# Optimization experiments

Measured on AMD Instinct MI355X. Metric: run time of the kernel, lower is better.

## Reference

```python
import jax, jax.numpy as jnp
import numpy as np

K = 8192      # codebook_dim
D = 256       # embedding_dim
BETA = 0.25
DECAY = 0.99
EPS = 1e-05


def setup_inputs() -> dict:
    key = jax.random.key(0)
    k1, k2, k3, k4 = jax.random.split(key, 4)
    lim = 1.0 / K
    return {
        "z": jax.random.normal(k1, (8, D, 32, 32), dtype=jnp.float32),
        "embedding": jax.random.uniform(k2, (K, D), minval=-lim, maxval=lim, dtype=jnp.float32),
        "cluster_size": jax.random.uniform(k3, (K,), dtype=jnp.float32),
        "ema_w": jax.random.uniform(k4, (K, D), minval=-lim, maxval=lim, dtype=jnp.float32),
    }


def reference(z, embedding, cluster_size, ema_w):
    # z: [B, C, H, W] -> [B, H, W, C]
    zp = jnp.transpose(z, (0, 2, 3, 1))
    zf = zp.reshape(-1, D)                                  # [N, D]
    # squared L2 distance to each code: ||z||^2 + ||e||^2 - 2 z.e
    d = (jnp.sum(zf * zf, axis=1, keepdims=True)
         + jnp.sum(embedding * embedding, axis=1)
         - 2.0 * jnp.einsum("nd,kd->nk", zf, embedding))    # [N, K]
    idx = jnp.argmin(d, axis=1)                             # [N]
    z_q = embedding[idx].reshape(zp.shape)                  # [B, H, W, C]

    # EMA update (training branch), expressed with segment sums instead of
    # materializing the one-hot [N, K] matrix.
    counts = jax.ops.segment_sum(jnp.ones_like(idx, dtype=zf.dtype), idx, num_segments=K)
    new_cs = cluster_size * DECAY + (1.0 - DECAY) * counts
    n = jnp.sum(new_cs)
    new_cs = (new_cs + EPS) / (n + K * EPS) * n
    dw = jax.ops.segment_sum(zf, idx, num_segments=K)       # encodings.T @ zf
    new_ema_w = ema_w * DECAY + (1.0 - DECAY) * dw
    new_embedding = new_ema_w / new_cs[:, None]

    sg = jax.lax.stop_gradient
    loss = jnp.mean((sg(z_q) - zp) ** 2) + BETA * jnp.mean((z_q - sg(zp)) ** 2)
    # straight-through estimator, back to NCHW
    z_q_out = jnp.transpose(zp + sg(z_q - zp), (0, 3, 1, 2))
    return z_q_out, loss, idx, new_cs, new_ema_w, new_embedding
```

## Files before the change

kernel.cpp:

```cpp
#include <hip/hip_runtime.h>

#define CHW 262144
#define HWD 1024

typedef _Float16 v8h __attribute__((ext_vector_type(8)));
typedef _Float16 v4h __attribute__((ext_vector_type(4)));
typedef float    v4f __attribute__((ext_vector_type(4)));

static const unsigned OFF_ASQ  = 0;
static const unsigned OFF_BSQ  = 8192;
static const unsigned OFF_CNT  = 16384;
static const unsigned OFF_HEAD = 24576;
static const unsigned OFF_NXT  = 32768;
static const unsigned OFF_SCAL = 40960;
static const unsigned OFF_AH   = 40968;
static const unsigned OFF_AM   = 1089544;
static const unsigned OFF_BH   = 2138120;
static const unsigned OFF_BM   = 3186696;

#define GLL(g, l) __builtin_amdgcn_global_load_lds( \
    (const __attribute__((address_space(1))) void*)(g), \
    (__attribute__((address_space(3))) void*)(l), 16, 0, 0)

__global__ __launch_bounds__(256) void k_prep(const float* __restrict__ z,
        const float* __restrict__ emb, float* __restrict__ asq, float* __restrict__ bsq,
        _Float16* __restrict__ Bh, _Float16* __restrict__ Bm,
        _Float16* __restrict__ Ah, _Float16* __restrict__ Am,
        float* __restrict__ zerobase) {
    int bx = blockIdx.x;
    int t = threadIdx.x;
    if (bx < 32) {
        int n = bx * 256 + t;
        const float* p = z + (size_t)(n >> 10) * CHW + (n & 1023);
        float s = 0.f;
        #pragma unroll 8
        for (int c = 0; c < 256; ++c) { float v = p[(size_t)c << 10]; s = fmaf(v, v, s); }
        asq[n] = s;
    } else if (bx < 2080) {
        int w = (bx - 32) * 4 + (t >> 6);
        int lane = t & 63;
        float4 v = *(const float4*)(emb + (size_t)w * 256 + lane * 4);
        float s = v.x * v.x;
        s = fmaf(v.y, v.y, s); s = fmaf(v.z, v.z, s); s = fmaf(v.w, v.w, s);
        #pragma unroll
        for (int m = 1; m < 64; m <<= 1) s += __shfl_xor(s, m, 64);
        if (lane == 0) bsq[w] = s;
        float e0 = v.x * 8192.0f, e1 = v.y * 8192.0f, e2 = v.z * 8192.0f, e3 = v.w * 8192.0f;
        _Float16 h0 = (_Float16)e0, h1 = (_Float16)e1, h2 = (_Float16)e2, h3 = (_Float16)e3;
        v4h hv = {h0, h1, h2, h3};
        v4h mv = {(_Float16)((e0 - (float)h0) * 2048.0f),
                  (_Float16)((e1 - (float)h1) * 2048.0f),
                  (_Float16)((e2 - (float)h2) * 2048.0f),
                  (_Float16)((e3 - (float)h3) * 2048.0f)};
        *(v4h*)(Bh + (size_t)w * 256 + lane * 4) = hv;
        *(v4h*)(Bm + (size_t)w * 256 + lane * 4) = mv;
    } else if (bx < 2592) {
        __shared__ float s[64][65];
        int blk = bx - 2080;
        int hw0 = (blk & 15) * 64;
        int c0  = ((blk >> 4) & 3) * 64;
        int b   = blk >> 6;
        #pragma unroll
        for (int ii = 0; ii < 16; ++ii) {
            int e = t + ii * 256;
            int c = e >> 6, x = e & 63;
            s[c][x] = z[(size_t)b * CHW + (size_t)(c0 + c) * HWD + hw0 + x];
        }
        __syncthreads();
        int n = t & 63, cseg = (t >> 6) * 16;
        _Float16 hbuf[16], mbuf[16];
        #pragma unroll
        for (int j = 0; j < 16; ++j) {
            float v = s[cseg + j][n];
            _Float16 h = (_Float16)v;
            float r = v - (float)h;
            hbuf[j] = h;
            mbuf[j] = (_Float16)(r * 2048.0f);
        }
        size_t off = ((size_t)b * 1024 + hw0 + n) * 256 + c0 + cseg;
        *(v8h*)(Ah + off)     = *(v8h*)(hbuf);
        *(v8h*)(Ah + off + 8) = *(v8h*)(hbuf + 8);
        *(v8h*)(Am + off)     = *(v8h*)(mbuf);
        *(v8h*)(Am + off + 8) = *(v8h*)(mbuf + 8);
    } else {
        int idx = (bx - 2592) * 1024 + t * 4;
        *(float4*)(zerobase + idx) = (float4){0.f, 0.f, 0.f, 0.f};
        if (bx == 2592 && t == 0)
            *(float4*)(zerobase + 24576) = (float4){0.f, 0.f, 0.f, 0.f};
    }
}

__global__ __launch_bounds__(512, 4) void k_main(
        const _Float16* __restrict__ Ah, const _Float16* __restrict__ Am,
        const _Float16* __restrict__ Bh, const _Float16* __restrict__ Bm,
        const float* __restrict__ asq, const float* __restrict__ bsq,
        unsigned* __restrict__ pdk) {
    __shared__ _Float16 lds[32768];
    const int kt = blockIdx.x, nt = blockIdx.y;
    const int n0 = nt * 128, k0 = kt * 128;
    const int t = threadIdx.x;
    const int lane = t & 63, w = t >> 6;
    const int wrow = w >> 1, wcol = w & 1;
    const int lm = lane & 15, quad = lane >> 4;

    v4f acc1[2][4], acc2[2][4];
    #pragma unroll
    for (int i = 0; i < 2; ++i)
        #pragma unroll
        for (int j = 0; j < 4; ++j) { acc1[i][j] = (v4f){0.f,0.f,0.f,0.f}; acc2[i][j] = (v4f){0.f,0.f,0.f,0.f}; }

    const int row0 = t >> 2;
    const int c40 = (t & 3) ^ ((row0 >> 1) & 3);
    const char* gA  = (const char*)Ah + (size_t)(n0 + row0) * 512 + c40 * 16;
    const char* gAm = (const char*)Am + (size_t)(n0 + row0) * 512 + c40 * 16;
    const char* gB  = (const char*)Bh + (size_t)(k0 + row0) * 512 + c40 * 16;
    const char* gBm = (const char*)Bm + (size_t)(k0 + row0) * 512 + c40 * 16;

    int sa[2], sb[4];
    #pragma unroll
    for (int i = 0; i < 2; ++i) {
        int mr = wrow * 32 + i * 16 + lm;
        sa[i] = mr * 32 + ((quad ^ ((mr >> 1) & 3)) * 8);
    }
    #pragma unroll
    for (int j = 0; j < 4; ++j) {
        int nr = wcol * 64 + j * 16 + lm;
        sb[j] = nr * 32 + ((quad ^ ((nr >> 1) & 3)) * 8);
    }

    auto stage = [&](int cb, int buf) {
        const size_t co = (size_t)cb * 64;
        _Float16* l = lds + buf * 16384 + t * 8;
        GLL(gA + co,  l);
        GLL(gAm + co, l + 4096);
        GLL(gB + co,  l + 8192);
        GLL(gBm + co, l + 12288);
    };

    stage(0, 0);
    for (int cb = 0; cb < 8; ++cb) {
        __syncthreads();
        if (cb < 7) stage(cb + 1, (cb + 1) & 1);
        const _Float16* L = lds + (cb & 1) * 16384;

        v8h fa[2], fam[2];
        #pragma unroll
        for (int i = 0; i < 2; ++i) {
            fa[i]  = *(const v8h*)(L + sa[i]);
            fam[i] = *(const v8h*)(L + 4096 + sa[i]);
        }
        #pragma unroll
        for (int jh = 0; jh < 2; ++jh) {
            v8h fb0  = *(const v8h*)(L + 8192 + sb[jh * 2]);
            v8h fb1  = *(const v8h*)(L + 8192 + sb[jh * 2 + 1]);
            v8h fbm0 = *(const v8h*)(L + 12288 + sb[jh * 2]);
            v8h fbm1 = *(const v8h*)(L + 12288 + sb[jh * 2 + 1]);
            #pragma unroll
            for (int i = 0; i < 2; ++i) {
                int j0 = jh * 2;
                acc1[i][j0]     = __builtin_amdgcn_mfma_f32_16x16x32_f16(fa[i],  fb0,  acc1[i][j0], 0, 0, 0);
                acc2[i][j0]     = __builtin_amdgcn_mfma_f32_16x16x32_f16(fa[i],  fbm0, acc2[i][j0], 0, 0, 0);
                acc2[i][j0]     = __builtin_amdgcn_mfma_f32_16x16x32_f16(fam[i], fb0,  acc2[i][j0], 0, 0, 0);
                acc1[i][j0 + 1] = __builtin_amdgcn_mfma_f32_16x16x32_f16(fa[i],  fb1,  acc1[i][j0 + 1], 0, 0, 0);
                acc2[i][j0 + 1] = __builtin_amdgcn_mfma_f32_16x16x32_f16(fa[i],  fbm1, acc2[i][j0 + 1], 0, 0, 0);
                acc2[i][j0 + 1] = __builtin_amdgcn_mfma_f32_16x16x32_f16(fam[i], fb1,  acc2[i][j0 + 1], 0, 0, 0);
            }
        }
    }

    float bvv[4];
    #pragma unroll
    for (int j = 0; j < 4; ++j) bvv[j] = bsq[k0 + wcol * 64 + j * 16 + lm];
    __syncthreads();
    unsigned* lrow = (unsigned*)lds;
    #pragma unroll
    for (int i = 0; i < 2; ++i) {
        #pragma unroll
        for (int r = 0; r < 4; ++r) {
            int mm = wrow * 32 + i * 16 + quad * 4 + r;
            float av_ = asq[n0 + mm];
            unsigned best = 0xFFFFFFFFu;
            #pragma unroll
            for (int j = 0; j < 4; ++j) {
                float S = fmaf(acc2[i][j][r], 4.8828125e-4f, acc1[i][j][r]) * 1.220703125e-4f;
                float dd = (av_ + bvv[j]) - 2.0f * S;
                float gv = dd - av_;
                int mi = (int)(gv * 65536.0f) + 32768;
                int col = k0 + wcol * 64 + j * 16 + lm;
                unsigned key = ((unsigned)mi << 13) | (unsigned)col;
                best = key < best ? key : best;
            }
            #pragma unroll
            for (int xm = 1; xm < 16; xm <<= 1) {
                unsigned o = __shfl_xor(best, xm, 64);
                best = o < best ? o : best;
            }
            if (lm == 0) lrow[wcol * 128 + mm] = best;
        }
    }
    __syncthreads();
    if (t < 256) pdk[(((size_t)nt * 128 + kt * 2) << 7) + t] = lrow[t];
}

__global__ __launch_bounds__(256) void k_zqr(const unsigned* __restrict__ pdk,
        const float* __restrict__ z, const float* __restrict__ emb, const float* __restrict__ cs,
        float* __restrict__ out_idx, int* __restrict__ cnt,
        int* __restrict__ head, int* __restrict__ nxt,
        float* __restrict__ out_zq, float* __restrict__ scal) {
    const int bx = blockIdx.x, by = blockIdx.y;
    const int n0 = bx * 64, c00 = by * 64;
    const int lane = threadIdx.x & 63, g = threadIdx.x >> 6;
    const int nt = bx >> 1, mb = (bx & 1) * 64;

    unsigned mn = 0xFFFFFFFFu;
    const unsigned* base = pdk + (((size_t)nt * 128 + g * 32) << 7) + mb + lane;
    #pragma unroll 8
    for (int jj = 0; jj < 32; ++jj) {
        unsigned key = base[jj << 7];
        mn = key < mn ? key : mn;
    }
    __shared__ unsigned part[4][64];
    part[g][lane] = mn;
    __syncthreads();
    unsigned k0v = part[0][lane], k1v = part[1][lane];
    unsigned k2v = part[2][lane], k3v = part[3][lane];
    unsigned f01 = k0v < k1v ? k0v : k1v;
    unsigned f23 = k2v < k3v ? k2v : k3v;
    unsigned fkey = f01 < f23 ? f01 : f23;
    int idxn = (int)(fkey & 8191u);
    int n = n0 + lane;

    if (by == 0) {
        if (g == 0) {
            out_idx[n] = (float)idxn;
            atomicAdd(cnt + idxn, 1);
            int old = atomicExch(head + idxn, n + 1);
            nxt[n] = old;
        } else if (g == 1) {
            float cv = cs[n];
            #pragma unroll
            for (int m = 1; m < 64; m <<= 1) cv += __shfl_xor(cv, m, 64);
            if (lane == 0) atomicAdd(scal + 1, cv);
        }
    }

    int b = n >> 10, hw = n & 1023;
    const float* zr = z + (size_t)b * CHW + hw;
    const float* er = emb + (size_t)idxn * 256;
    float* oz = out_zq + (size_t)b * CHW + hw;
    float ls = 0.f;
    #pragma unroll
    for (int q = 0; q < 4; ++q) {
        int c = c00 + g * 16 + q * 4;
        float4 e4 = *(const float4*)(er + c);
        float ev[4] = {e4.x, e4.y, e4.z, e4.w};
        #pragma unroll
        for (int r = 0; r < 4; ++r) {
            float zp = zr[(size_t)(c + r) << 10];
            float dif = ev[r] - zp;
            oz[(size_t)(c + r) << 10] = zp + dif;
            ls = fmaf(dif, dif, ls);
        }
    }
    #pragma unroll
    for (int m = 1; m < 64; m <<= 1) ls += __shfl_xor(ls, m, 64);
    __shared__ float red[4];
    if (lane == 0) red[g] = ls;
    __syncthreads();
    if (threadIdx.x == 0) atomicAdd(scal, red[0] + red[1] + red[2] + red[3]);
}

__global__ __launch_bounds__(256) void k_fin(const float* __restrict__ cs, const float* __restrict__ ema,
        const int* __restrict__ head, const int* __restrict__ nxt,
        const _Float16* __restrict__ Ah, const _Float16* __restrict__ Am,
        const float* __restrict__ scal, const int* __restrict__ cnt,
        float* __restrict__ out_ncs, float* __restrict__ out_ema,
        float* __restrict__ out_emb, float* __restrict__ out_loss) {
    int k = blockIdx.x * 4 + (threadIdx.x >> 6);
    int lane = threadIdx.x & 63;
    float4 dwv = {0.f, 0.f, 0.f, 0.f};
    int cur = head[k];
    while (cur) {
        int n = cur - 1;
        v4h hh = *(const v4h*)(Ah + (size_t)n * 256 + lane * 4);
        v4h mm = *(const v4h*)(Am + (size_t)n * 256 + lane * 4);
        dwv.x += fmaf((float)mm[0], 4.8828125e-4f, (float)hh[0]);
        dwv.y += fmaf((float)mm[1], 4.8828125e-4f, (float)hh[1]);
        dwv.z += fmaf((float)mm[2], 4.8828125e-4f, (float)hh[2]);
        dwv.w += fmaf((float)mm[3], 4.8828125e-4f, (float)hh[3]);
        cur = nxt[n];
    }
    const float C1 = (float)(1.0 - 0.99);
    const float KEPS = (float)(8192 * 1e-5);
    float ncs0v = cs[k] * 0.99f + C1 * (float)cnt[k];
    float nsum = 0.99f * scal[1] + C1 * 8192.0f;
    float ncs = (ncs0v + 1e-5f) / (nsum + KEPS) * nsum;
    if (lane == 0) out_ncs[k] = ncs;
    size_t base = (size_t)k * 256 + lane * 4;
    float4 e4 = *(const float4*)(ema + base);
    float r0 = e4.x * 0.99f + C1 * dwv.x;
    float r1 = e4.y * 0.99f + C1 * dwv.y;
    float r2 = e4.z * 0.99f + C1 * dwv.z;
    float r3 = e4.w * 0.99f + C1 * dwv.w;
    out_ema[base + 0] = r0; out_ema[base + 1] = r1; out_ema[base + 2] = r2; out_ema[base + 3] = r3;
    out_emb[base + 0] = r0 / ncs; out_emb[base + 1] = r1 / ncs;
    out_emb[base + 2] = r2 / ncs; out_emb[base + 3] = r3 / ncs;
    if (blockIdx.x == 0 && threadIdx.x == 0) {
        float m = scal[0] * (1.0f / 2097152.0f);
        out_loss[0] = m + 0.25f * m;
    }
}

extern "C" void kernel_launch(void* const* d_in, const int* in_sizes, int n_in,
                              void* d_out, int out_size, void* d_ws, size_t ws_size,
                              hipStream_t stream) {
    const float* z   = (const float*)d_in[0];
    const float* emb = (const float*)d_in[1];
    const float* cs  = (const float*)d_in[2];
    const float* ema = (const float*)d_in[3];
    float* out = (float*)d_out;
    float* wsf = (float*)d_ws;

    float* asq  = wsf + OFF_ASQ;
    float* bsq  = wsf + OFF_BSQ;
    int*   cnt  = (int*)(wsf + OFF_CNT);
    int*   head = (int*)(wsf + OFF_HEAD);
    int*   nxt  = (int*)(wsf + OFF_NXT);
    float* scal = wsf + OFF_SCAL;
    _Float16* Ah = (_Float16*)(wsf + OFF_AH);
    _Float16* Am = (_Float16*)(wsf + OFF_AM);
    _Float16* Bh = (_Float16*)(wsf + OFF_BH);
    _Float16* Bm = (_Float16*)(wsf + OFF_BM);

    float* out_zq   = out;
    float* out_loss = out + 2097152;
    float* out_idx  = out + 2097153;
    float* out_ncs  = out + 2105345;
    float* out_ema  = out + 2113537;
    float* out_emb  = out + 4210689;

    unsigned* pdk = (unsigned*)(out + 2113540);

    k_prep<<<2608, 256, 0, stream>>>(z, emb, asq, bsq, Bh, Bm, Ah, Am, wsf + OFF_CNT);
    k_main<<<dim3(64, 64), 512, 0, stream>>>(Ah, Am, Bh, Bm, asq, bsq, pdk);
    k_zqr<<<dim3(128, 4), 256, 0, stream>>>(pdk, z, emb, cs, out_idx, cnt, head, nxt, out_zq, scal);
    k_fin<<<2048, 256, 0, stream>>>(cs, ema, head, nxt, Ah, Am, scal, cnt, out_ncs, out_ema, out_emb, out_loss);
}
```

Measured before the change: 242.3 us.

## Halve k_main block to 4 waves with 64x64 per-wave tiles

Cuts k_main from 512 to 256 threads per 128x128 tile, so each wave computes a 64x64 sub-tile (4x4 MFMA fragments) instead of 32x64. Each thread now issues two global-to-LDS loads per operand. The change raises register reuse of A/B fragments per LDS read and cuts LDS traffic per FLOP. It also swaps __syncthreads for an explicit vmcnt wait plus barrier, and adds sched_barrier/setprio grouping to interleave LDS reads with MFMA bursts. The cost is more accumulator registers and fewer waves per CU to hide latency.

```diff
diff --git a/kernel.cpp b/kernel.cpp
--- a/kernel.cpp
+++ b/kernel.cpp
@@ -90,7 +90,7 @@
     }
 }
 
-__global__ __launch_bounds__(512, 4) void k_main(
+__global__ __launch_bounds__(256, 2) void k_main(
         const _Float16* __restrict__ Ah, const _Float16* __restrict__ Am,
         const _Float16* __restrict__ Bh, const _Float16* __restrict__ Bm,
         const float* __restrict__ asq, const float* __restrict__ bsq,
@@ -103,9 +103,9 @@
     const int wrow = w >> 1, wcol = w & 1;
     const int lm = lane & 15, quad = lane >> 4;
 
-    v4f acc1[2][4], acc2[2][4];
-    #pragma unroll
-    for (int i = 0; i < 2; ++i)
+    v4f acc1[4][4], acc2[4][4];
+    #pragma unroll
+    for (int i = 0; i < 4; ++i)
         #pragma unroll
         for (int j = 0; j < 4; ++j) { acc1[i][j] = (v4f){0.f,0.f,0.f,0.f}; acc2[i][j] = (v4f){0.f,0.f,0.f,0.f}; }
 
@@ -116,10 +116,10 @@
     const char* gB  = (const char*)Bh + (size_t)(k0 + row0) * 512 + c40 * 16;
     const char* gBm = (const char*)Bm + (size_t)(k0 + row0) * 512 + c40 * 16;
 
-    int sa[2], sb[4];
-    #pragma unroll
-    for (int i = 0; i < 2; ++i) {
-        int mr = wrow * 32 + i * 16 + lm;
+    int sa[4], sb[4];
+    #pragma unroll
+    for (int i = 0; i < 4; ++i) {
+        int mr = wrow * 64 + i * 16 + lm;
         sa[i] = mr * 32 + ((quad ^ ((mr >> 1) & 3)) * 8);
     }
     #pragma unroll
@@ -131,42 +131,81 @@
     auto stage = [&](int cb, int buf) {
         const size_t co = (size_t)cb * 64;
         _Float16* l = lds + buf * 16384 + t * 8;
-        GLL(gA + co,  l);
-        GLL(gAm + co, l + 4096);
-        GLL(gB + co,  l + 8192);
-        GLL(gBm + co, l + 12288);
+        GLL(gA + co,           l);
+        GLL(gA + co + 32768,   l + 2048);
+        GLL(gAm + co,          l + 4096);
+        GLL(gAm + co + 32768,  l + 6144);
+        GLL(gB + co,           l + 8192);
+        GLL(gB + co + 32768,   l + 10240);
+        GLL(gBm + co,          l + 12288);
+        GLL(gBm + co + 32768,  l + 14336);
     };
+
+#define MFMA16(A, B, C) __builtin_amdgcn_mfma_f32_16x16x32_f16(A, B, C, 0, 0, 0)
+#define PROD(I, J, FA, FAM, FB, FBM) do { \
+        acc1[I][J] = MFMA16(FA,  FB,  acc1[I][J]); \
+        acc2[I][J] = MFMA16(FA,  FBM, acc2[I][J]); \
+        acc2[I][J] = MFMA16(FAM, FB,  acc2[I][J]); \
+    } while (0)
 
     stage(0, 0);
     for (int cb = 0; cb < 8; ++cb) {
-        __syncthreads();
+        asm volatile("s_waitcnt vmcnt(0)" ::: "memory");
+        __builtin_amdgcn_s_barrier();
+        __builtin_amdgcn_sched_barrier(0);
         if (cb < 7) stage(cb + 1, (cb + 1) & 1);
         const _Float16* L = lds + (cb & 1) * 16384;
 
-        v8h fa[2], fam[2];
-        #pragma unroll
-        for (int i = 0; i < 2; ++i) {
-            fa[i]  = *(const v8h*)(L + sa[i]);
-            fam[i] = *(const v8h*)(L + 4096 + sa[i]);
-        }
-        #pragma unroll
-        for (int jh = 0; jh < 2; ++jh) {
-            v8h fb0  = *(const v8h*)(L + 8192 + sb[jh * 2]);
-            v8h fb1  = *(const v8h*)(L + 8192 + sb[jh * 2 + 1]);
-            v8h fbm0 = *(const v8h*)(L + 12288 + sb[jh * 2]);
-            v8h fbm1 = *(const v8h*)(L + 12288 + sb[jh * 2 + 1]);
-            #pragma unroll
-            for (int i = 0; i < 2; ++i) {
-                int j0 = jh * 2;
-                acc1[i][j0]     = __builtin_amdgcn_mfma_f32_16x16x32_f16(fa[i],  fb0,  acc1[i][j0], 0, 0, 0);
-                acc2[i][j0]     = __builtin_amdgcn_mfma_f32_16x16x32_f16(fa[i],  fbm0, acc2[i][j0], 0, 0, 0);
-                acc2[i][j0]     = __builtin_amdgcn_mfma_f32_16x16x32_f16(fam[i], fb0,  acc2[i][j0], 0, 0, 0);
-                acc1[i][j0 + 1] = __builtin_amdgcn_mfma_f32_16x16x32_f16(fa[i],  fb1,  acc1[i][j0 + 1], 0, 0, 0);
-                acc2[i][j0 + 1] = __builtin_amdgcn_mfma_f32_16x16x32_f16(fa[i],  fbm1, acc2[i][j0 + 1], 0, 0, 0);
-                acc2[i][j0 + 1] = __builtin_amdgcn_mfma_f32_16x16x32_f16(fam[i], fb1,  acc2[i][j0 + 1], 0, 0, 0);
-            }
-        }
-    }
+        v8h fa0  = *(const v8h*)(L + sa[0]);
+        v8h fa1  = *(const v8h*)(L + sa[1]);
+        v8h fam0 = *(const v8h*)(L + 4096 + sa[0]);
+        v8h fam1 = *(const v8h*)(L + 4096 + sa[1]);
+        v8h fb0  = *(const v8h*)(L + 8192 + sb[0]);
+        v8h fb1  = *(const v8h*)(L + 8192 + sb[1]);
+        v8h fbm0 = *(const v8h*)(L + 12288 + sb[0]);
+        v8h fbm1 = *(const v8h*)(L + 12288 + sb[1]);
+        __builtin_amdgcn_s_setprio(1);
+        PROD(0, 0, fa0, fam0, fb0, fbm0);
+        PROD(0, 1, fa0, fam0, fb1, fbm1);
+        PROD(1, 0, fa1, fam1, fb0, fbm0);
+        PROD(1, 1, fa1, fam1, fb1, fbm1);
+        __builtin_amdgcn_s_setprio(0);
+        __builtin_amdgcn_sched_barrier(0);
+
+        v8h fa2  = *(const v8h*)(L + sa[2]);
+        v8h fa3  = *(const v8h*)(L + sa[3]);
+        v8h fam2 = *(const v8h*)(L + 4096 + sa[2]);
+        v8h fam3 = *(const v8h*)(L + 4096 + sa[3]);
+        __builtin_amdgcn_s_setprio(1);
+        PROD(2, 0, fa2, fam2, fb0, fbm0);
+        PROD(2, 1, fa2, fam2, fb1, fbm1);
+        PROD(3, 0, fa3, fam3, fb0, fbm0);
+        PROD(3, 1, fa3, fam3, fb1, fbm1);
+        __builtin_amdgcn_s_setprio(0);
+        __builtin_amdgcn_sched_barrier(0);
+
+        v8h fb2  = *(const v8h*)(L + 8192 + sb[2]);
+        v8h fb3  = *(const v8h*)(L + 8192 + sb[3]);
+        v8h fbm2 = *(const v8h*)(L + 12288 + sb[2]);
+        v8h fbm3 = *(const v8h*)(L + 12288 + sb[3]);
+        __builtin_amdgcn_s_setprio(1);
+        PROD(0, 2, fa0, fam0, fb2, fbm2);
+        PROD(0, 3, fa0, fam0, fb3, fbm3);
+        PROD(1, 2, fa1, fam1, fb2, fbm2);
+        PROD(1, 3, fa1, fam1, fb3, fbm3);
+        __builtin_amdgcn_s_setprio(0);
+        __builtin_amdgcn_sched_barrier(0);
+
+        __builtin_amdgcn_s_setprio(1);
+        PROD(2, 2, fa2, fam2, fb2, fbm2);
+        PROD(2, 3, fa2, fam2, fb3, fbm3);
+        PROD(3, 2, fa3, fam3, fb2, fbm2);
+        PROD(3, 3, fa3, fam3, fb3, fbm3);
+        __builtin_amdgcn_s_setprio(0);
+        __builtin_amdgcn_sched_barrier(0);
+    }
+#undef PROD
+#undef MFMA16
 
     float bvv[4];
     #pragma unroll
@@ -174,10 +213,10 @@
     __syncthreads();
     unsigned* lrow = (unsigned*)lds;
     #pragma unroll
-    for (int i = 0; i < 2; ++i) {
+    for (int i = 0; i < 4; ++i) {
         #pragma unroll
         for (int r = 0; r < 4; ++r) {
-            int mm = wrow * 32 + i * 16 + quad * 4 + r;
+            int mm = wrow * 64 + i * 16 + quad * 4 + r;
             float av_ = asq[n0 + mm];
             unsigned best = 0xFFFFFFFFu;
             #pragma unroll
@@ -342,7 +381,7 @@
     unsigned* pdk = (unsigned*)(out + 2113540);
 
     k_prep<<<2608, 256, 0, stream>>>(z, emb, asq, bsq, Bh, Bm, Ah, Am, wsf + OFF_CNT);
-    k_main<<<dim3(64, 64), 512, 0, stream>>>(Ah, Am, Bh, Bm, asq, bsq, pdk);
+    k_main<<<dim3(64, 64), 256, 0, stream>>>(Ah, Am, Bh, Bm, asq, bsq, pdk);
     k_zqr<<<dim3(128, 4), 256, 0, stream>>>(pdk, z, emb, cs, out_idx, cnt, head, nxt, out_zq, scal);
     k_fin<<<2048, 256, 0, stream>>>(cs, ema, head, nxt, Ah, Am, scal, cnt, out_ncs, out_ema, out_emb, out_loss);
 }
```

Result: no change. 247.1 us (+2.0%).

## Load MFMA fragments directly from global memory into registers, dropping LDS staging

Applied to the files above, without the earlier changes.

Replaces the LDS double-buffered staging in the distance GEMM with direct per-wave global loads of MFMA fragments into registers, software-pipelining the B fragments across K chunks. Blocks shrink to 256 threads, and each wave computes a 64x64 sub-tile with twice the accumulators. This removes LDS traffic and block-wide barriers in the main loop. In exchange it loses the sharing of staged tiles across waves, increases global/L2 reads, and raises register pressure.

```diff
diff --git a/kernel.cpp b/kernel.cpp
--- a/kernel.cpp
+++ b/kernel.cpp
@@ -17,10 +17,6 @@
 static const unsigned OFF_AM   = 1089544;
 static const unsigned OFF_BH   = 2138120;
 static const unsigned OFF_BM   = 3186696;
-
-#define GLL(g, l) __builtin_amdgcn_global_load_lds( \
-    (const __attribute__((address_space(1))) void*)(g), \
-    (__attribute__((address_space(3))) void*)(l), 16, 0, 0)
 
 __global__ __launch_bounds__(256) void k_prep(const float* __restrict__ z,
         const float* __restrict__ emb, float* __restrict__ asq, float* __restrict__ bsq,
@@ -90,12 +86,12 @@
     }
 }
 
-__global__ __launch_bounds__(512, 4) void k_main(
+__global__ __launch_bounds__(256, 2) void k_main(
         const _Float16* __restrict__ Ah, const _Float16* __restrict__ Am,
         const _Float16* __restrict__ Bh, const _Float16* __restrict__ Bm,
         const float* __restrict__ asq, const float* __restrict__ bsq,
         unsigned* __restrict__ pdk) {
-    __shared__ _Float16 lds[32768];
+    __shared__ unsigned lrow[256];
     const int kt = blockIdx.x, nt = blockIdx.y;
     const int n0 = nt * 128, k0 = kt * 128;
     const int t = threadIdx.x;
@@ -103,81 +99,88 @@
     const int wrow = w >> 1, wcol = w & 1;
     const int lm = lane & 15, quad = lane >> 4;
 
-    v4f acc1[2][4], acc2[2][4];
-    #pragma unroll
-    for (int i = 0; i < 2; ++i)
+    v4f acc1[4][4], acc2[4][4];
+    #pragma unroll
+    for (int i = 0; i < 4; ++i)
         #pragma unroll
         for (int j = 0; j < 4; ++j) { acc1[i][j] = (v4f){0.f,0.f,0.f,0.f}; acc2[i][j] = (v4f){0.f,0.f,0.f,0.f}; }
 
-    const int row0 = t >> 2;
-    const int c40 = (t & 3) ^ ((row0 >> 1) & 3);
-    const char* gA  = (const char*)Ah + (size_t)(n0 + row0) * 512 + c40 * 16;
-    const char* gAm = (const char*)Am + (size_t)(n0 + row0) * 512 + c40 * 16;
-    const char* gB  = (const char*)Bh + (size_t)(k0 + row0) * 512 + c40 * 16;
-    const char* gBm = (const char*)Bm + (size_t)(k0 + row0) * 512 + c40 * 16;
-
-    int sa[2], sb[4];
-    #pragma unroll
-    for (int i = 0; i < 2; ++i) {
-        int mr = wrow * 32 + i * 16 + lm;
-        sa[i] = mr * 32 + ((quad ^ ((mr >> 1) & 3)) * 8);
-    }
-    #pragma unroll
-    for (int j = 0; j < 4; ++j) {
-        int nr = wcol * 64 + j * 16 + lm;
-        sb[j] = nr * 32 + ((quad ^ ((nr >> 1) & 3)) * 8);
-    }
-
-    auto stage = [&](int cb, int buf) {
-        const size_t co = (size_t)cb * 64;
-        _Float16* l = lds + buf * 16384 + t * 8;
-        GLL(gA + co,  l);
-        GLL(gAm + co, l + 4096);
-        GLL(gB + co,  l + 8192);
-        GLL(gBm + co, l + 12288);
-    };
-
-    stage(0, 0);
-    for (int cb = 0; cb < 8; ++cb) {
-        __syncthreads();
-        if (cb < 7) stage(cb + 1, (cb + 1) & 1);
-        const _Float16* L = lds + (cb & 1) * 16384;
-
-        v8h fa[2], fam[2];
-        #pragma unroll
-        for (int i = 0; i < 2; ++i) {
-            fa[i]  = *(const v8h*)(L + sa[i]);
-            fam[i] = *(const v8h*)(L + 4096 + sa[i]);
-        }
-        #pragma unroll
-        for (int jh = 0; jh < 2; ++jh) {
-            v8h fb0  = *(const v8h*)(L + 8192 + sb[jh * 2]);
-            v8h fb1  = *(const v8h*)(L + 8192 + sb[jh * 2 + 1]);
-            v8h fbm0 = *(const v8h*)(L + 12288 + sb[jh * 2]);
-            v8h fbm1 = *(const v8h*)(L + 12288 + sb[jh * 2 + 1]);
-            #pragma unroll
-            for (int i = 0; i < 2; ++i) {
-                int j0 = jh * 2;
-                acc1[i][j0]     = __builtin_amdgcn_mfma_f32_16x16x32_f16(fa[i],  fb0,  acc1[i][j0], 0, 0, 0);
-                acc2[i][j0]     = __builtin_amdgcn_mfma_f32_16x16x32_f16(fa[i],  fbm0, acc2[i][j0], 0, 0, 0);
-                acc2[i][j0]     = __builtin_amdgcn_mfma_f32_16x16x32_f16(fam[i], fb0,  acc2[i][j0], 0, 0, 0);
-                acc1[i][j0 + 1] = __builtin_amdgcn_mfma_f32_16x16x32_f16(fa[i],  fb1,  acc1[i][j0 + 1], 0, 0, 0);
-                acc2[i][j0 + 1] = __builtin_amdgcn_mfma_f32_16x16x32_f16(fa[i],  fbm1, acc2[i][j0 + 1], 0, 0, 0);
-                acc2[i][j0 + 1] = __builtin_amdgcn_mfma_f32_16x16x32_f16(fam[i], fb1,  acc2[i][j0 + 1], 0, 0, 0);
-            }
-        }
-    }
+    const char* pA  = (const char*)Ah + (size_t)(n0 + wrow * 64 + lm) * 512 + quad * 16;
+    const char* pAm = (const char*)Am + (size_t)(n0 + wrow * 64 + lm) * 512 + quad * 16;
+    const char* pB  = (const char*)Bh + (size_t)(k0 + wcol * 64 + lm) * 512 + quad * 16;
+    const char* pBm = (const char*)Bm + (size_t)(k0 + wcol * 64 + lm) * 512 + quad * 16;
+
+#define LOADA(FA, FAM, CB) do { \
+        _Pragma("unroll") \
+        for (int i_ = 0; i_ < 4; ++i_) { \
+            FA[i_]  = *(const v8h*)(pA  + (size_t)i_ * 8192 + (CB) * 64); \
+            FAM[i_] = *(const v8h*)(pAm + (size_t)i_ * 8192 + (CB) * 64); \
+        } } while (0)
+#define LOADB(FB, FBM, CB) do { \
+        _Pragma("unroll") \
+        for (int j_ = 0; j_ < 4; ++j_) { \
+            FB[j_]  = *(const v8h*)(pB  + (size_t)j_ * 8192 + (CB) * 64); \
+            FBM[j_] = *(const v8h*)(pBm + (size_t)j_ * 8192 + (CB) * 64); \
+        } } while (0)
+
+#define MFMA16(A, B, C) __builtin_amdgcn_mfma_f32_16x16x32_f16(A, B, C, 0, 0, 0)
+#define PROD(I, J, FA, FAM, FB, FBM) do { \
+        acc1[I][J] = MFMA16(FA,  FB,  acc1[I][J]); \
+        acc2[I][J] = MFMA16(FA,  FBM, acc2[I][J]); \
+        acc2[I][J] = MFMA16(FAM, FB,  acc2[I][J]); \
+    } while (0)
+#define COMPUTE(FA, FAM, FB, FBM) do { \
+        PROD(0, 0, FA[0], FAM[0], FB[0], FBM[0]); \
+        PROD(0, 1, FA[0], FAM[0], FB[1], FBM[1]); \
+        PROD(1, 0, FA[1], FAM[1], FB[0], FBM[0]); \
+        PROD(1, 1, FA[1], FAM[1], FB[1], FBM[1]); \
+        PROD(2, 0, FA[2], FAM[2], FB[0], FBM[0]); \
+        PROD(2, 1, FA[2], FAM[2], FB[1], FBM[1]); \
+        PROD(3, 0, FA[3], FAM[3], FB[0], FBM[0]); \
+        PROD(3, 1, FA[3], FAM[3], FB[1], FBM[1]); \
+        PROD(0, 2, FA[0], FAM[0], FB[2], FBM[2]); \
+        PROD(0, 3, FA[0], FAM[0], FB[3], FBM[3]); \
+        PROD(1, 2, FA[1], FAM[1], FB[2], FBM[2]); \
+        PROD(1, 3, FA[1], FAM[1], FB[3], FBM[3]); \
+        PROD(2, 2, FA[2], FAM[2], FB[2], FBM[2]); \
+        PROD(2, 3, FA[2], FAM[2], FB[3], FBM[3]); \
+        PROD(3, 2, FA[3], FAM[3], FB[2], FBM[2]); \
+        PROD(3, 3, FA[3], FAM[3], FB[3], FBM[3]); \
+    } while (0)
+
+    v8h fb0[4], fbm0[4], fb1[4], fbm1[4];
+    LOADB(fb0, fbm0, 0);
+    #pragma unroll
+    for (int cbp = 0; cbp < 4; ++cbp) {
+        {
+            const int cb = cbp * 2;
+            v8h fa[4], fam[4];
+            LOADA(fa, fam, cb);
+            LOADB(fb1, fbm1, cb + 1);
+            COMPUTE(fa, fam, fb0, fbm0);
+        }
+        {
+            const int cb = cbp * 2 + 1;
+            v8h fa[4], fam[4];
+            LOADA(fa, fam, cb);
+            if (cb < 7) LOADB(fb0, fbm0, cb + 1);
+            COMPUTE(fa, fam, fb1, fbm1);
+        }
+    }
+#undef COMPUTE
+#undef PROD
+#undef MFMA16
+#undef LOADB
+#undef LOADA
 
     float bvv[4];
     #pragma unroll
     for (int j = 0; j < 4; ++j) bvv[j] = bsq[k0 + wcol * 64 + j * 16 + lm];
-    __syncthreads();
-    unsigned* lrow = (unsigned*)lds;
-    #pragma unroll
-    for (int i = 0; i < 2; ++i) {
+    #pragma unroll
+    for (int i = 0; i < 4; ++i) {
         #pragma unroll
         for (int r = 0; r < 4; ++r) {
-            int mm = wrow * 32 + i * 16 + quad * 4 + r;
+            int mm = wrow * 64 + i * 16 + quad * 4 + r;
             float av_ = asq[n0 + mm];
             unsigned best = 0xFFFFFFFFu;
             #pragma unroll
@@ -199,7 +202,7 @@
         }
     }
     __syncthreads();
-    if (t < 256) pdk[(((size_t)nt * 128 + kt * 2) << 7) + t] = lrow[t];
+    pdk[(((size_t)nt * 128 + kt * 2) << 7) + t] = lrow[t];
 }
 
 __global__ __launch_bounds__(256) void k_zqr(const unsigned* __restrict__ pdk,
@@ -342,7 +345,7 @@
     unsigned* pdk = (unsigned*)(out + 2113540);
 
     k_prep<<<2608, 256, 0, stream>>>(z, emb, asq, bsq, Bh, Bm, Ah, Am, wsf + OFF_CNT);
-    k_main<<<dim3(64, 64), 512, 0, stream>>>(Ah, Am, Bh, Bm, asq, bsq, pdk);
+    k_main<<<dim3(64, 64), 256, 0, stream>>>(Ah, Am, Bh, Bm, asq, bsq, pdk);
     k_zqr<<<dim3(128, 4), 256, 0, stream>>>(pdk, z, emb, cs, out_idx, cnt, head, nxt, out_zq, scal);
     k_fin<<<2048, 256, 0, stream>>>(cs, ema, head, nxt, Ah, Am, scal, cnt, out_ncs, out_ema, out_emb, out_loss);
 }
```

Result: slower. 372.0 us (+53.5%).

## Enlarge GEMM tiles to 256x256, merge split-fp16 accumulators, add XCD-aware block mapping

Applied to the files above, without the earlier changes.

The distance GEMM tile grows from 128x128 to 256x256 per workgroup with doubled LDS staging. Each loaded fragment is now reused across more MFMAs, which cuts global and LDS traffic per FLOP. The residual terms are no longer scaled by 2048, so high and residual products accumulate into a single accumulator instead of two. Blocks are remapped so neighbouring k-tiles share an XCD, and MFMA sections run at raised priority. The cost is higher register and LDS use (occupancy bound drops from 4 to 2) and possible fp16 underflow of the unscaled residuals, which could affect accuracy.

```diff
diff --git a/kernel.cpp b/kernel.cpp
--- a/kernel.cpp
+++ b/kernel.cpp
@@ -48,10 +48,10 @@
         float e0 = v.x * 8192.0f, e1 = v.y * 8192.0f, e2 = v.z * 8192.0f, e3 = v.w * 8192.0f;
         _Float16 h0 = (_Float16)e0, h1 = (_Float16)e1, h2 = (_Float16)e2, h3 = (_Float16)e3;
         v4h hv = {h0, h1, h2, h3};
-        v4h mv = {(_Float16)((e0 - (float)h0) * 2048.0f),
-                  (_Float16)((e1 - (float)h1) * 2048.0f),
-                  (_Float16)((e2 - (float)h2) * 2048.0f),
-                  (_Float16)((e3 - (float)h3) * 2048.0f)};
+        v4h mv = {(_Float16)(e0 - (float)h0),
+                  (_Float16)(e1 - (float)h1),
+                  (_Float16)(e2 - (float)h2),
+                  (_Float16)(e3 - (float)h3)};
         *(v4h*)(Bh + (size_t)w * 256 + lane * 4) = hv;
         *(v4h*)(Bm + (size_t)w * 256 + lane * 4) = mv;
     } else if (bx < 2592) {
@@ -75,7 +75,7 @@
             _Float16 h = (_Float16)v;
             float r = v - (float)h;
             hbuf[j] = h;
-            mbuf[j] = (_Float16)(r * 2048.0f);
+            mbuf[j] = (_Float16)r;
         }
         size_t off = ((size_t)b * 1024 + hw0 + n) * 256 + c0 + cseg;
         *(v8h*)(Ah + off)     = *(v8h*)(hbuf);
@@ -90,24 +90,27 @@
     }
 }
 
-__global__ __launch_bounds__(512, 4) void k_main(
+__global__ __launch_bounds__(512, 2) void k_main(
         const _Float16* __restrict__ Ah, const _Float16* __restrict__ Am,
         const _Float16* __restrict__ Bh, const _Float16* __restrict__ Bm,
         const float* __restrict__ asq, const float* __restrict__ bsq,
         unsigned* __restrict__ pdk) {
-    __shared__ _Float16 lds[32768];
-    const int kt = blockIdx.x, nt = blockIdx.y;
-    const int n0 = nt * 128, k0 = kt * 128;
+    __shared__ _Float16 lds[65536];
+    const int bid = blockIdx.x;
+    const int xcd = bid & 7, sblk = bid >> 3;
+    const int kt = xcd * 4 + (sblk & 3);
+    const int nt = sblk >> 2;
+    const int n0 = nt * 256, k0 = kt * 256;
     const int t = threadIdx.x;
     const int lane = t & 63, w = t >> 6;
     const int wrow = w >> 1, wcol = w & 1;
     const int lm = lane & 15, quad = lane >> 4;
 
-    v4f acc1[2][4], acc2[2][4];
-    #pragma unroll
-    for (int i = 0; i < 2; ++i)
-        #pragma unroll
-        for (int j = 0; j < 4; ++j) { acc1[i][j] = (v4f){0.f,0.f,0.f,0.f}; acc2[i][j] = (v4f){0.f,0.f,0.f,0.f}; }
+    v4f acc[4][8];
+    #pragma unroll
+    for (int i = 0; i < 4; ++i)
+        #pragma unroll
+        for (int j = 0; j < 8; ++j) acc[i][j] = (v4f){0.f,0.f,0.f,0.f};
 
     const int row0 = t >> 2;
     const int c40 = (t & 3) ^ ((row0 >> 1) & 3);
@@ -116,90 +119,113 @@
     const char* gB  = (const char*)Bh + (size_t)(k0 + row0) * 512 + c40 * 16;
     const char* gBm = (const char*)Bm + (size_t)(k0 + row0) * 512 + c40 * 16;
 
-    int sa[2], sb[4];
-    #pragma unroll
-    for (int i = 0; i < 2; ++i) {
-        int mr = wrow * 32 + i * 16 + lm;
+    int sa[4], sb[8];
+    #pragma unroll
+    for (int i = 0; i < 4; ++i) {
+        int mr = wrow * 64 + i * 16 + lm;
         sa[i] = mr * 32 + ((quad ^ ((mr >> 1) & 3)) * 8);
     }
     #pragma unroll
-    for (int j = 0; j < 4; ++j) {
-        int nr = wcol * 64 + j * 16 + lm;
+    for (int j = 0; j < 8; ++j) {
+        int nr = wcol * 128 + j * 16 + lm;
         sb[j] = nr * 32 + ((quad ^ ((nr >> 1) & 3)) * 8);
     }
 
-    auto stage = [&](int cb, int buf) {
-        const size_t co = (size_t)cb * 64;
-        _Float16* l = lds + buf * 16384 + t * 8;
-        GLL(gA + co,  l);
-        GLL(gAm + co, l + 4096);
-        GLL(gB + co,  l + 8192);
-        GLL(gBm + co, l + 12288);
+    auto stage = [&](int s, int buf) {
+        const size_t co = (size_t)s * 64;
+        _Float16* l = lds + buf * 32768 + t * 8;
+        GLL(gA + co,           l);
+        GLL(gA + co + 65536,   l + 4096);
+        GLL(gAm + co,          l + 8192);
+        GLL(gAm + co + 65536,  l + 12288);
+        GLL(gB + co,           l + 16384);
+        GLL(gB + co + 65536,   l + 20480);
+        GLL(gBm + co,          l + 24576);
+        GLL(gBm + co + 65536,  l + 28672);
     };
 
+#define MFMA16(A, B, C) __builtin_amdgcn_mfma_f32_16x16x32_f16(A, B, C, 0, 0, 0)
+
     stage(0, 0);
-    for (int cb = 0; cb < 8; ++cb) {
-        __syncthreads();
-        if (cb < 7) stage(cb + 1, (cb + 1) & 1);
-        const _Float16* L = lds + (cb & 1) * 16384;
-
-        v8h fa[2], fam[2];
-        #pragma unroll
-        for (int i = 0; i < 2; ++i) {
+    for (int s = 0; s < 8; ++s) {
+        asm volatile("s_waitcnt vmcnt(0)" ::: "memory");
+        __builtin_amdgcn_s_barrier();
+        __builtin_amdgcn_sched_barrier(0);
+        if (s < 7) stage(s + 1, (s + 1) & 1);
+        const _Float16* L = lds + (s & 1) * 32768;
+
+        v8h fa[4], fam[4];
+        #pragma unroll
+        for (int i = 0; i < 4; ++i) {
             fa[i]  = *(const v8h*)(L + sa[i]);
-            fam[i] = *(const v8h*)(L + 4096 + sa[i]);
+            fam[i] = *(const v8h*)(L + 8192 + sa[i]);
         }
         #pragma unroll
         for (int jh = 0; jh < 2; ++jh) {
-            v8h fb0  = *(const v8h*)(L + 8192 + sb[jh * 2]);
-            v8h fb1  = *(const v8h*)(L + 8192 + sb[jh * 2 + 1]);
-            v8h fbm0 = *(const v8h*)(L + 12288 + sb[jh * 2]);
-            v8h fbm1 = *(const v8h*)(L + 12288 + sb[jh * 2 + 1]);
+            v8h fb[4], fbm[4];
             #pragma unroll
-            for (int i = 0; i < 2; ++i) {
-                int j0 = jh * 2;
-                acc1[i][j0]     = __builtin_amdgcn_mfma_f32_16x16x32_f16(fa[i],  fb0,  acc1[i][j0], 0, 0, 0);
-                acc2[i][j0]     = __builtin_amdgcn_mfma_f32_16x16x32_f16(fa[i],  fbm0, acc2[i][j0], 0, 0, 0);
-                acc2[i][j0]     = __builtin_amdgcn_mfma_f32_16x16x32_f16(fam[i], fb0,  acc2[i][j0], 0, 0, 0);
-                acc1[i][j0 + 1] = __builtin_amdgcn_mfma_f32_16x16x32_f16(fa[i],  fb1,  acc1[i][j0 + 1], 0, 0, 0);
-                acc2[i][j0 + 1] = __builtin_amdgcn_mfma_f32_16x16x32_f16(fa[i],  fbm1, acc2[i][j0 + 1], 0, 0, 0);
-                acc2[i][j0 + 1] = __builtin_amdgcn_mfma_f32_16x16x32_f16(fam[i], fb1,  acc2[i][j0 + 1], 0, 0, 0);
+            for (int j4 = 0; j4 < 4; ++j4) {
+                fb[j4]  = *(const v8h*)(L + 16384 + sb[jh * 4 + j4]);
+                fbm[j4] = *(const v8h*)(L + 24576 + sb[jh * 4 + j4]);
             }
-        }
-    }
-
-    float bvv[4];
-    #pragma unroll
-    for (int j = 0; j < 4; ++j) bvv[j] = bsq[k0 + wcol * 64 + j * 16 + lm];
+            __builtin_amdgcn_s_setprio(1);
+            #pragma unroll
+            for (int i = 0; i < 4; ++i) {
+                #pragma unroll
+                for (int j4 = 0; j4 < 4; ++j4) {
+                    const int j = jh * 4 + j4;
+                    acc[i][j] = MFMA16(fa[i],  fb[j4],  acc[i][j]);
+                    acc[i][j] = MFMA16(fa[i],  fbm[j4], acc[i][j]);
+                    acc[i][j] = MFMA16(fam[i], fb[j4],  acc[i][j]);
+                }
+            }
+            __builtin_amdgcn_s_setprio(0);
+        }
+    }
+#undef MFMA16
+
+    float bvv[8];
+    #pragma unroll
+    for (int j = 0; j < 8; ++j) bvv[j] = bsq[k0 + wcol * 128 + j * 16 + lm];
     __syncthreads();
     unsigned* lrow = (unsigned*)lds;
     #pragma unroll
-    for (int i = 0; i < 2; ++i) {
+    for (int i = 0; i < 4; ++i) {
         #pragma unroll
         for (int r = 0; r < 4; ++r) {
-            int mm = wrow * 32 + i * 16 + quad * 4 + r;
+            int mm = wrow * 64 + i * 16 + quad * 4 + r;
             float av_ = asq[n0 + mm];
-            unsigned best = 0xFFFFFFFFu;
             #pragma unroll
-            for (int j = 0; j < 4; ++j) {
-                float S = fmaf(acc2[i][j][r], 4.8828125e-4f, acc1[i][j][r]) * 1.220703125e-4f;
-                float dd = (av_ + bvv[j]) - 2.0f * S;
-                float gv = dd - av_;
-                int mi = (int)(gv * 65536.0f) + 32768;
-                int col = k0 + wcol * 64 + j * 16 + lm;
-                unsigned key = ((unsigned)mi << 13) | (unsigned)col;
-                best = key < best ? key : best;
+            for (int jh = 0; jh < 2; ++jh) {
+                unsigned best = 0xFFFFFFFFu;
+                #pragma unroll
+                for (int j4 = 0; j4 < 4; ++j4) {
+                    const int j = jh * 4 + j4;
+                    float S = acc[i][j][r] * 1.220703125e-4f;
+                    float dd = (av_ + bvv[j]) - 2.0f * S;
+                    float gv = dd - av_;
+                    int mi = (int)(gv * 65536.0f) + 32768;
+                    int col = k0 + wcol * 128 + j * 16 + lm;
+                    unsigned key = ((unsigned)mi << 13) | (unsigned)col;
+                    best = key < best ? key : best;
+                }
+                #pragma unroll
+                for (int xm = 1; xm < 16; xm <<= 1) {
+                    unsigned o = __shfl_xor(best, xm, 64);
+                    best = o < best ? o : best;
+                }
+                if (lm == 0)
+                    lrow[(mm >> 7) * 512 + (wcol * 2 + jh) * 128 + (mm & 127)] = best;
             }
-            #pragma unroll
-            for (int xm = 1; xm < 16; xm <<= 1) {
-                unsigned o = __shfl_xor(best, xm, 64);
-                best = o < best ? o : best;
-            }
-            if (lm == 0) lrow[wcol * 128 + mm] = best;
         }
     }
     __syncthreads();
-    if (t < 256) pdk[(((size_t)nt * 128 + kt * 2) << 7) + t] = lrow[t];
+    #pragma unroll
+    for (int u = 0; u < 2; ++u) {
+        int e = t + u * 512;
+        pdk[((size_t)(nt * 2 + (e >> 9)) * 128 + kt * 4 + ((e >> 7) & 3)) * 128 + (e & 127)]
+            = lrow[e];
+    }
 }
 
 __global__ __launch_bounds__(256) void k_zqr(const unsigned* __restrict__ pdk,
@@ -284,10 +310,10 @@
         int n = cur - 1;
         v4h hh = *(const v4h*)(Ah + (size_t)n * 256 + lane * 4);
         v4h mm = *(const v4h*)(Am + (size_t)n * 256 + lane * 4);
-        dwv.x += fmaf((float)mm[0], 4.8828125e-4f, (float)hh[0]);
-        dwv.y += fmaf((float)mm[1], 4.8828125e-4f, (float)hh[1]);
-        dwv.z += fmaf((float)mm[2], 4.8828125e-4f, (float)hh[2]);
-        dwv.w += fmaf((float)mm[3], 4.8828125e-4f, (float)hh[3]);
+        dwv.x += (float)hh[0] + (float)mm[0];
+        dwv.y += (float)hh[1] + (float)mm[1];
+        dwv.z += (float)hh[2] + (float)mm[2];
+        dwv.w += (float)hh[3] + (float)mm[3];
         cur = nxt[n];
     }
     const float C1 = (float)(1.0 - 0.99);
@@ -342,7 +368,7 @@
     unsigned* pdk = (unsigned*)(out + 2113540);
 
     k_prep<<<2608, 256, 0, stream>>>(z, emb, asq, bsq, Bh, Bm, Ah, Am, wsf + OFF_CNT);
-    k_main<<<dim3(64, 64), 512, 0, stream>>>(Ah, Am, Bh, Bm, asq, bsq, pdk);
+    k_main<<<1024, 512, 0, stream>>>(Ah, Am, Bh, Bm, asq, bsq, pdk);
     k_zqr<<<dim3(128, 4), 256, 0, stream>>>(pdk, z, emb, cs, out_idx, cnt, head, nxt, out_zq, scal);
     k_fin<<<2048, 256, 0, stream>>>(cs, ema, head, nxt, Ah, Am, scal, cnt, out_ncs, out_ema, out_emb, out_loss);
 }
```

After: 230.6 us. 1.05x faster.
